# Kernel optimization log

Measured on AMD Instinct MI355X. Metric: run time of the kernel, lower is better.

## Reference

```python
import jax, jax.numpy as jnp
import numpy as np

B, N, D_MEM, D_HID = 64, 65536, 1024, 1024


def setup_inputs() -> dict:
    key = jax.random.key(0)
    k1, k2, k3 = jax.random.split(key, 3)
    memory_bank = jax.random.normal(k1, (N, D_MEM), dtype=jnp.float32)
    decoder_state = jax.random.normal(k2, (B, D_HID), dtype=jnp.float32)
    # nn.Linear(memory_bank_size -> hidden_size, bias=False): weight [D_HID, D_MEM]
    W = jax.random.normal(k3, (D_HID, D_MEM), dtype=jnp.float32) / np.sqrt(D_MEM)
    # ragged tree sizes summing exactly to N (concrete, built on host)
    rng = np.random.default_rng(0)
    lens = rng.integers(512, 1536, size=B).astype(np.float64)
    lens = np.maximum(1, np.floor(lens * N / lens.sum()).astype(np.int64))
    lens[-1] += N - lens.sum()
    return {
        "memory_bank": memory_bank,
        "decoder_state": decoder_state,
        "W": W,
        "tree_node_num_lst": jnp.asarray(lens, dtype=jnp.int64),
    }


def reference(memory_bank, decoder_state, W, tree_node_num_lst):
    # segment id per node: tree index it belongs to (total_repeat_length keeps it jit-able)
    n_total = memory_bank.shape[0]
    batch = decoder_state.shape[0]
    seg = jnp.repeat(jnp.arange(batch), tree_node_num_lst, total_repeat_length=n_total)  # [N]
    # memory_project: one big GEMM instead of per-tree launches
    enc = memory_bank @ W.T                                  # [N, D_HID]
    # per-node score = <decoder_state[tree], enc[node]>
    scores = jnp.sum(enc * decoder_state[seg], axis=-1)      # [N]
    # segment (per-tree) stable softmax
    m = jax.ops.segment_max(scores, seg, num_segments=batch)  # [B]
    e = jnp.exp(scores - m[seg])                              # [N]
    z = jax.ops.segment_sum(e, seg, num_segments=batch)       # [B]
    attn = e / z[seg]                                         # [N]
    # context = attn-weighted sum of raw memory bank per tree
    context = jax.ops.segment_sum(attn[:, None] * memory_bank, seg, num_segments=batch)  # [B, D_MEM]
    return context
```

## Files before the change

kernel.cpp:

```cpp
#include <hip/hip_runtime.h>
#include <hip/hip_bf16.h>
#include <math.h>

#define B_TREES 64
#define N_NODES 65536
#define D 1024
#define D4 (D/4)
#define PIECE 16
#define MAXP (N_NODES/PIECE + B_TREES)

__global__ void setup_kernel(const int* __restrict__ lens32,
                             int* __restrict__ off, int* __restrict__ pbase) {
    if (threadIdx.x == 0 && blockIdx.x == 0) {
        long long s32 = 0;
        for (int b = 0; b < B_TREES; ++b) s32 += lens32[b];
        const bool is32 = (s32 == (long long)N_NODES);
        int acc = 0, pacc = 0;
        off[0] = 0; pbase[0] = 0;
        for (int b = 0; b < B_TREES; ++b) {
            int len = is32 ? lens32[b] : (int)(((const long long*)lens32)[b]);
            acc  += len;
            pacc += (len + PIECE - 1) / PIECE;
            off[b + 1]   = acc;
            pbase[b + 1] = pacc;
        }
    }
}

__global__ void pieces_kernel(const int* __restrict__ off, const int* __restrict__ pbase,
                              int* __restrict__ pseg, int* __restrict__ pstart,
                              int* __restrict__ plen) {
    const int b  = blockIdx.x;
    const int s0 = off[b], s1 = off[b + 1];
    const int np = pbase[b + 1] - pbase[b];
    for (int i = threadIdx.x; i < np; i += blockDim.x) {
        int st = s0 + i * PIECE;
        int p  = pbase[b] + i;
        pseg[p]   = b;
        pstart[p] = st;
        plen[p]   = min(PIECE, s1 - st);
    }
}

__global__ void v_kernel(const float* __restrict__ ds, const float* __restrict__ W,
                         float* __restrict__ v) {
    const int m  = blockIdx.x * 256 + threadIdx.x;
    const int b0 = blockIdx.y * 4;
    const int h0 = blockIdx.z * 128;
    float acc[4] = {0.f, 0.f, 0.f, 0.f};
    for (int h = h0; h < h0 + 128; ++h) {
        float wv = W[h * D + m];
        #pragma unroll
        for (int j = 0; j < 4; ++j)
            acc[j] += ds[(b0 + j) * D + h] * wv;
    }
    #pragma unroll
    for (int j = 0; j < 4; ++j)
        atomicAdd(&v[(b0 + j) * D + m], acc[j]);
}

__global__ __launch_bounds__(256) void fused_kernel(
        const float4* __restrict__ mb, const float4* __restrict__ v,
        const int* __restrict__ pseg, const int* __restrict__ pstart,
        const int* __restrict__ plen, const int* __restrict__ pbase,
        float* __restrict__ pm, float* __restrict__ pz, float4* __restrict__ pctx) {
    const int wave = threadIdx.x >> 6;
    const int lane = threadIdx.x & 63;
    const int p    = blockIdx.x * 4 + wave;
    if (p >= pbase[B_TREES]) return;

    const int seg = pseg[p];
    const int s0  = pstart[p];
    const int ln  = plen[p];

    const float4* vrow = v + (size_t)seg * D4;
    const float4 v0 = vrow[lane], v1 = vrow[64 + lane],
                 v2 = vrow[128 + lane], v3 = vrow[192 + lane];

    float4 a0 = make_float4(0.f,0.f,0.f,0.f), a1 = a0, a2 = a0, a3 = a0;
    float rm = -INFINITY, rz = 0.f;

    for (int i = 0; i < ln; ++i) {
        const float4* mrow = mb + (size_t)(s0 + i) * D4;
        const float4 m0 = mrow[lane],       m1 = mrow[64 + lane],
                     m2 = mrow[128 + lane], m3 = mrow[192 + lane];
        float d0 = m0.x*v0.x + m0.y*v0.y + m0.z*v0.z + m0.w*v0.w;
        float d1 = m1.x*v1.x + m1.y*v1.y + m1.z*v1.z + m1.w*v1.w;
        float d2 = m2.x*v2.x + m2.y*v2.y + m2.z*v2.z + m2.w*v2.w;
        float d3 = m3.x*v3.x + m3.y*v3.y + m3.z*v3.z + m3.w*v3.w;
        float d  = (d0 + d1) + (d2 + d3);
        #pragma unroll
        for (int o = 32; o > 0; o >>= 1) d += __shfl_xor(d, o, 64);

        const float nm = fmaxf(rm, d);
        const float sc = __expf(rm - nm);
        const float w  = __expf(d - nm);
        a0.x = a0.x*sc + w*m0.x; a0.y = a0.y*sc + w*m0.y;
        a0.z = a0.z*sc + w*m0.z; a0.w = a0.w*sc + w*m0.w;
        a1.x = a1.x*sc + w*m1.x; a1.y = a1.y*sc + w*m1.y;
        a1.z = a1.z*sc + w*m1.z; a1.w = a1.w*sc + w*m1.w;
        a2.x = a2.x*sc + w*m2.x; a2.y = a2.y*sc + w*m2.y;
        a2.z = a2.z*sc + w*m2.z; a2.w = a2.w*sc + w*m2.w;
        a3.x = a3.x*sc + w*m3.x; a3.y = a3.y*sc + w*m3.y;
        a3.z = a3.z*sc + w*m3.z; a3.w = a3.w*sc + w*m3.w;
        rz = rz*sc + w;
        rm = nm;
    }

    if (lane == 0) { pm[p] = rm; pz[p] = rz; }
    float4* o = pctx + (size_t)p * D4;
    o[lane] = a0; o[64 + lane] = a1; o[128 + lane] = a2; o[192 + lane] = a3;
}

__global__ void finalize_kernel(const int* __restrict__ pbase,
                                const float* __restrict__ pm, const float* __restrict__ pz,
                                const float4* __restrict__ pctx, float4* __restrict__ out) {
    const int b  = blockIdx.x;
    const int t  = threadIdx.x;
    const int q0 = pbase[b], q1 = pbase[b + 1];

    float mb_ = -INFINITY;
    for (int q = q0; q < q1; ++q) mb_ = fmaxf(mb_, pm[q]);
    float zb = 0.f;
    for (int q = q0; q < q1; ++q) zb += pz[q] * __expf(pm[q] - mb_);
    const float inv = 1.f / zb;

    float4 acc = make_float4(0.f,0.f,0.f,0.f);
    for (int q = q0; q < q1; ++q) {
        const float s = __expf(pm[q] - mb_);
        const float4 c = pctx[(size_t)q * D4 + t];
        acc.x += s * c.x; acc.y += s * c.y; acc.z += s * c.z; acc.w += s * c.w;
    }
    acc.x *= inv; acc.y *= inv; acc.z *= inv; acc.w *= inv;
    out[(size_t)b * D4 + t] = acc;
}

extern "C" void kernel_launch(void* const* d_in, const int* in_sizes, int n_in,
                              void* d_out, int out_size, void* d_ws, size_t ws_size,
                              hipStream_t stream) {
    const float* mb   = (const float*)d_in[0];
    const float* ds   = (const float*)d_in[1];
    const float* W    = (const float*)d_in[2];
    const int*   lens = (const int*)d_in[3];
    float*       out  = (float*)d_out;

    char* ws = (char*)d_ws;
    int*   off    = (int*)(ws + 0);
    int*   pbase  = (int*)(ws + 512);
    float* v      = (float*)(ws + 1024);
    int*   pseg   = (int*)(ws + 1024 + 262144);
    int*   pstart = (int*)(ws + 1024 + 262144 + 32768);
    int*   plen   = (int*)(ws + 1024 + 262144 + 65536);
    float* pm     = (float*)(ws + 1024 + 262144 + 98304);
    float* pz     = (float*)(ws + 1024 + 262144 + 131072);
    float4* pctx  = (float4*)(ws + 1024 + 262144 + 163840);

    hipMemsetAsync(v, 0, 64 * D * sizeof(float), stream);

    setup_kernel<<<1, 64, 0, stream>>>(lens, off, pbase);
    pieces_kernel<<<B_TREES, 256, 0, stream>>>(off, pbase, pseg, pstart, plen);

    {
        dim3 grid(4, 16, 8);
        v_kernel<<<grid, 256, 0, stream>>>(ds, W, v);
    }

    fused_kernel<<<(MAXP + 3) / 4, 256, 0, stream>>>(
        (const float4*)mb, (const float4*)v, pseg, pstart, plen, pbase,
        pm, pz, pctx);

    finalize_kernel<<<B_TREES, 256, 0, stream>>>(
        pbase, pm, pz, pctx, (float4*)out);
}
```

Baseline: 442.0 us.

## Merge setup and pieces kernels; process two rows per iteration in fused kernel

```diff
diff --git a/kernel.cpp b/kernel.cpp
--- a/kernel.cpp
+++ b/kernel.cpp
@@ -10,35 +10,55 @@
 #define MAXP (N_NODES/PIECE + B_TREES)
 
 __global__ void setup_kernel(const int* __restrict__ lens32,
-                             int* __restrict__ off, int* __restrict__ pbase) {
-    if (threadIdx.x == 0 && blockIdx.x == 0) {
-        long long s32 = 0;
-        for (int b = 0; b < B_TREES; ++b) s32 += lens32[b];
-        const bool is32 = (s32 == (long long)N_NODES);
-        int acc = 0, pacc = 0;
-        off[0] = 0; pbase[0] = 0;
-        for (int b = 0; b < B_TREES; ++b) {
-            int len = is32 ? lens32[b] : (int)(((const long long*)lens32)[b]);
-            acc  += len;
-            pacc += (len + PIECE - 1) / PIECE;
-            off[b + 1]   = acc;
-            pbase[b + 1] = pacc;
-        }
-    }
-}
-
-__global__ void pieces_kernel(const int* __restrict__ off, const int* __restrict__ pbase,
-                              int* __restrict__ pseg, int* __restrict__ pstart,
-                              int* __restrict__ plen) {
-    const int b  = blockIdx.x;
-    const int s0 = off[b], s1 = off[b + 1];
-    const int np = pbase[b + 1] - pbase[b];
-    for (int i = threadIdx.x; i < np; i += blockDim.x) {
-        int st = s0 + i * PIECE;
-        int p  = pbase[b] + i;
-        pseg[p]   = b;
+                             int* __restrict__ off, int* __restrict__ pbase,
+                             int* __restrict__ pseg, int* __restrict__ pstart,
+                             int* __restrict__ plen) {
+    __shared__ int sh_off[B_TREES + 1];
+    __shared__ int sh_pb[B_TREES + 1];
+
+    const int t = threadIdx.x;
+    if (t < 64) {
+        const int lane = t;
+        int l32 = lens32[lane];
+        int s = l32;
+        #pragma unroll
+        for (int o = 32; o > 0; o >>= 1) s += __shfl_xor(s, o, 64);
+        const bool is32 = (s == N_NODES);
+        int len = is32 ? l32 : (int)(((const long long*)lens32)[lane]);
+        int scan = len;
+        #pragma unroll
+        for (int o = 1; o < 64; o <<= 1) {
+            int u = __shfl_up(scan, o, 64);
+            if (lane >= o) scan += u;
+        }
+        int pc = (len + PIECE - 1) / PIECE;
+        int pscan = pc;
+        #pragma unroll
+        for (int o = 1; o < 64; o <<= 1) {
+            int u = __shfl_up(pscan, o, 64);
+            if (lane >= o) pscan += u;
+        }
+        sh_off[lane + 1] = scan;
+        sh_pb[lane + 1]  = pscan;
+        if (lane == 0) { sh_off[0] = 0; sh_pb[0] = 0; }
+        off[lane + 1]   = scan;
+        pbase[lane + 1] = pscan;
+        if (lane == 0) { off[0] = 0; pbase[0] = 0; }
+    }
+    __syncthreads();
+
+    const int total = sh_pb[B_TREES];
+    for (int p = t; p < total; p += 256) {
+        int lo = 0, hi = B_TREES - 1;
+        while (lo < hi) {
+            int mid = (lo + hi + 1) >> 1;
+            if (sh_pb[mid] <= p) lo = mid; else hi = mid - 1;
+        }
+        const int i  = p - sh_pb[lo];
+        const int st = sh_off[lo] + i * PIECE;
+        pseg[p]   = lo;
         pstart[p] = st;
-        plen[p]   = min(PIECE, s1 - st);
+        plen[p]   = min(PIECE, sh_off[lo + 1] - st);
     }
 }
 
@@ -80,31 +100,70 @@
     float4 a0 = make_float4(0.f,0.f,0.f,0.f), a1 = a0, a2 = a0, a3 = a0;
     float rm = -INFINITY, rz = 0.f;
 
-    for (int i = 0; i < ln; ++i) {
-        const float4* mrow = mb + (size_t)(s0 + i) * D4;
-        const float4 m0 = mrow[lane],       m1 = mrow[64 + lane],
-                     m2 = mrow[128 + lane], m3 = mrow[192 + lane];
-        float d0 = m0.x*v0.x + m0.y*v0.y + m0.z*v0.z + m0.w*v0.w;
-        float d1 = m1.x*v1.x + m1.y*v1.y + m1.z*v1.z + m1.w*v1.w;
-        float d2 = m2.x*v2.x + m2.y*v2.y + m2.z*v2.z + m2.w*v2.w;
-        float d3 = m3.x*v3.x + m3.y*v3.y + m3.z*v3.z + m3.w*v3.w;
-        float d  = (d0 + d1) + (d2 + d3);
-        #pragma unroll
-        for (int o = 32; o > 0; o >>= 1) d += __shfl_xor(d, o, 64);
-
-        const float nm = fmaxf(rm, d);
-        const float sc = __expf(rm - nm);
-        const float w  = __expf(d - nm);
-        a0.x = a0.x*sc + w*m0.x; a0.y = a0.y*sc + w*m0.y;
-        a0.z = a0.z*sc + w*m0.z; a0.w = a0.w*sc + w*m0.w;
-        a1.x = a1.x*sc + w*m1.x; a1.y = a1.y*sc + w*m1.y;
-        a1.z = a1.z*sc + w*m1.z; a1.w = a1.w*sc + w*m1.w;
-        a2.x = a2.x*sc + w*m2.x; a2.y = a2.y*sc + w*m2.y;
-        a2.z = a2.z*sc + w*m2.z; a2.w = a2.w*sc + w*m2.w;
-        a3.x = a3.x*sc + w*m3.x; a3.y = a3.y*sc + w*m3.y;
-        a3.z = a3.z*sc + w*m3.z; a3.w = a3.w*sc + w*m3.w;
-        rz = rz*sc + w;
-        rm = nm;
+    const float4* base = mb + (size_t)s0 * D4;
+
+    if (ln == PIECE) {
+        #pragma unroll 2
+        for (int i = 0; i < PIECE; i += 2) {
+            const float4* rA = base + (size_t)i * D4;
+            const float4* rB = rA + D4;
+            const float4 A0 = rA[lane],       A1 = rA[64 + lane],
+                         A2 = rA[128 + lane], A3 = rA[192 + lane];
+            const float4 B0 = rB[lane],       B1 = rB[64 + lane],
+                         B2 = rB[128 + lane], B3 = rB[192 + lane];
+            float dA = (A0.x*v0.x + A0.y*v0.y + A0.z*v0.z + A0.w*v0.w)
+                     + (A1.x*v1.x + A1.y*v1.y + A1.z*v1.z + A1.w*v1.w)
+                     + (A2.x*v2.x + A2.y*v2.y + A2.z*v2.z + A2.w*v2.w)
+                     + (A3.x*v3.x + A3.y*v3.y + A3.z*v3.z + A3.w*v3.w);
+            float dB = (B0.x*v0.x + B0.y*v0.y + B0.z*v0.z + B0.w*v0.w)
+                     + (B1.x*v1.x + B1.y*v1.y + B1.z*v1.z + B1.w*v1.w)
+                     + (B2.x*v2.x + B2.y*v2.y + B2.z*v2.z + B2.w*v2.w)
+                     + (B3.x*v3.x + B3.y*v3.y + B3.z*v3.z + B3.w*v3.w);
+            #pragma unroll
+            for (int o = 32; o > 0; o >>= 1) {
+                dA += __shfl_xor(dA, o, 64);
+                dB += __shfl_xor(dB, o, 64);
+            }
+            const float nm = fmaxf(rm, fmaxf(dA, dB));
+            const float sc = __expf(rm - nm);
+            const float wA = __expf(dA - nm);
+            const float wB = __expf(dB - nm);
+            a0.x = a0.x*sc + wA*A0.x + wB*B0.x; a0.y = a0.y*sc + wA*A0.y + wB*B0.y;
+            a0.z = a0.z*sc + wA*A0.z + wB*B0.z; a0.w = a0.w*sc + wA*A0.w + wB*B0.w;
+            a1.x = a1.x*sc + wA*A1.x + wB*B1.x; a1.y = a1.y*sc + wA*A1.y + wB*B1.y;
+            a1.z = a1.z*sc + wA*A1.z + wB*B1.z; a1.w = a1.w*sc + wA*A1.w + wB*B1.w;
+            a2.x = a2.x*sc + wA*A2.x + wB*B2.x; a2.y = a2.y*sc + wA*A2.y + wB*B2.y;
+            a2.z = a2.z*sc + wA*A2.z + wB*B2.z; a2.w = a2.w*sc + wA*A2.w + wB*B2.w;
+            a3.x = a3.x*sc + wA*A3.x + wB*B3.x; a3.y = a3.y*sc + wA*A3.y + wB*B3.y;
+            a3.z = a3.z*sc + wA*A3.z + wB*B3.z; a3.w = a3.w*sc + wA*A3.w + wB*B3.w;
+            rz = rz*sc + wA + wB;
+            rm = nm;
+        }
+    } else {
+        for (int i = 0; i < ln; ++i) {
+            const float4* mrow = base + (size_t)i * D4;
+            const float4 m0 = mrow[lane],       m1 = mrow[64 + lane],
+                         m2 = mrow[128 + lane], m3 = mrow[192 + lane];
+            float d = (m0.x*v0.x + m0.y*v0.y + m0.z*v0.z + m0.w*v0.w)
+                    + (m1.x*v1.x + m1.y*v1.y + m1.z*v1.z + m1.w*v1.w)
+                    + (m2.x*v2.x + m2.y*v2.y + m2.z*v2.z + m2.w*v2.w)
+                    + (m3.x*v3.x + m3.y*v3.y + m3.z*v3.z + m3.w*v3.w);
+            #pragma unroll
+            for (int o = 32; o > 0; o >>= 1) d += __shfl_xor(d, o, 64);
+            const float nm = fmaxf(rm, d);
+            const float sc = __expf(rm - nm);
+            const float w  = __expf(d - nm);
+            a0.x = a0.x*sc + w*m0.x; a0.y = a0.y*sc + w*m0.y;
+            a0.z = a0.z*sc + w*m0.z; a0.w = a0.w*sc + w*m0.w;
+            a1.x = a1.x*sc + w*m1.x; a1.y = a1.y*sc + w*m1.y;
+            a1.z = a1.z*sc + w*m1.z; a1.w = a1.w*sc + w*m1.w;
+            a2.x = a2.x*sc + w*m2.x; a2.y = a2.y*sc + w*m2.y;
+            a2.z = a2.z*sc + w*m2.z; a2.w = a2.w*sc + w*m2.w;
+            a3.x = a3.x*sc + w*m3.x; a3.y = a3.y*sc + w*m3.y;
+            a3.z = a3.z*sc + w*m3.z; a3.w = a3.w*sc + w*m3.w;
+            rz = rz*sc + w;
+            rm = nm;
+        }
     }
 
     if (lane == 0) { pm[p] = rm; pz[p] = rz; }
@@ -157,8 +216,7 @@
 
     hipMemsetAsync(v, 0, 64 * D * sizeof(float), stream);
 
-    setup_kernel<<<1, 64, 0, stream>>>(lens, off, pbase);
-    pieces_kernel<<<B_TREES, 256, 0, stream>>>(off, pbase, pseg, pstart, plen);
+    setup_kernel<<<1, 256, 0, stream>>>(lens, off, pbase, pseg, pstart, plen);
 
     {
         dim3 grid(4, 16, 8);
```

After: 437.8 us. No clear change (-0.9%).
